# Kernel tuning notes

Hardware: AMD Instinct MI355X
Metric: run time of the kernel (lower is better)

The kernel has to match this reference:

```python
import jax, jax.numpy as jnp
import numpy as np

TOPK = 10
NUM_CLASSES = 80
ALPHA = 0.5
BETA = 6.0
EPS = 1e-9


def setup_inputs() -> dict:
    key = jax.random.key(0)
    ks = jax.random.split(key, 7)
    bs, A, n, C = 16, 8400, 64, NUM_CLASSES
    pd_scores = jax.random.uniform(ks[0], (bs, A, C), jnp.float32)
    # valid xyxy boxes inside a 640x640 image
    pxy = jax.random.uniform(ks[1], (bs, A, 2), jnp.float32) * 576.0
    pwh = jax.random.uniform(ks[2], (bs, A, 2), jnp.float32) * 64.0 + 8.0
    pd_bboxes = jnp.concatenate([pxy, pxy + pwh], axis=-1)
    gxy = jax.random.uniform(ks[3], (bs, n, 2), jnp.float32) * 576.0
    gwh = jax.random.uniform(ks[4], (bs, n, 2), jnp.float32) * 64.0 + 8.0
    gt_bboxes = jnp.concatenate([gxy, gxy + gwh], axis=-1)
    anc_points = jax.random.uniform(ks[5], (A, 2), jnp.float32) * 640.0
    gt_labels = jax.random.randint(ks[6], (bs, n, 1), 0, C, dtype=jnp.int32)
    return {"pd_scores": pd_scores, "pd_bboxes": pd_bboxes,
            "anc_points": anc_points, "gt_labels": gt_labels,
            "gt_bboxes": gt_bboxes}


def _iou(gt_bboxes, pd_bboxes, eps=EPS):
    # gt_bboxes: (bs, n, 4), pd_bboxes: (bs, A, 4) -> (bs, n, A)
    b1 = gt_bboxes[:, :, None, :]
    b2 = pd_bboxes[:, None, :, :]
    lt = jnp.maximum(b1[..., :2], b2[..., :2])
    rb = jnp.minimum(b1[..., 2:], b2[..., 2:])
    overlap = jnp.clip(rb - lt, 0).prod(-1)
    area1 = jnp.clip(b1[..., 2:] - b1[..., :2], 0).prod(-1)
    area2 = jnp.clip(b2[..., 2:] - b2[..., :2], 0).prod(-1)
    return overlap / (area1 + area2 - overlap + eps)


def _assign(pd_scores, pd_bboxes, anc_points, gt_labels, gt_bboxes):
    bs, A, C = pd_scores.shape
    n = gt_bboxes.shape[1]
    dt = pd_scores.dtype
    labels = gt_labels[..., 0]                       # (bs, n)
    # ---- box metrics: gather class score per gt (bs, n, A) ----
    bi = jnp.arange(bs)[:, None]                     # (bs, 1)
    bbox_scores = pd_scores[bi, :, labels]           # (bs, n, A)
    overlaps = _iou(gt_bboxes, pd_bboxes)            # (bs, n, A)
    align_metric = bbox_scores ** ALPHA * overlaps ** BETA
    # ---- anchor-center-in-gt mask ----
    lt = gt_bboxes[..., None, :2]                    # (bs, n, 1, 2)
    rb = gt_bboxes[..., None, 2:]
    anc = anc_points[None, None]                     # (1, 1, A, 2)
    deltas_min = jnp.minimum((anc - lt).min(-1), (rb - anc).min(-1))
    mask_in_gts = (deltas_min > EPS).astype(dt)      # (bs, n, A)
    # ---- top-k candidates per gt (scatter-add instead of huge one-hot) ----
    metrics = align_metric * mask_in_gts
    topk_vals, topk_idxs = jax.lax.top_k(metrics, TOPK)
    valid = topk_vals.max(-1, keepdims=True) > EPS
    topk_idxs = jnp.where(valid, topk_idxs, 0)
    bi3 = jnp.arange(bs)[:, None, None]
    ni3 = jnp.arange(n)[None, :, None]
    cnt = jnp.zeros((bs, n, A), dt).at[bi3, ni3, topk_idxs].add(1.0)
    is_in_topk = jnp.where(cnt > 1, jnp.zeros((), dt), cnt)
    mask_pos = is_in_topk * mask_in_gts
    # ---- resolve anchors assigned to multiple gts via highest IoU ----
    fg_mask = mask_pos.sum(-2)                       # (bs, A)
    mask_multi = fg_mask[:, None, :] > 1             # (bs, 1->n, A)
    is_max = jax.nn.one_hot(overlaps.argmax(1), n, axis=1, dtype=dt)  # (bs, n, A)
    mask_pos = jnp.where(mask_multi, is_max, mask_pos)
    fg_mask = mask_pos.sum(-2)
    target_gt_idx = mask_pos.argmax(-2)              # (bs, A)
    # ---- gather targets ----
    flat_idx = target_gt_idx + jnp.arange(bs)[:, None] * n
    target_labels = jnp.maximum(labels.reshape(-1)[flat_idx], 0)
    target_bboxes = gt_bboxes.reshape(-1, 4)[flat_idx]
    target_scores = jax.nn.one_hot(target_labels, C, dtype=dt)
    target_scores = jnp.where(fg_mask[..., None] > 0, target_scores,
                              jnp.zeros((), dt))
    # ---- normalize scores by task-aligned metric ----
    align_metric = align_metric * mask_pos
    pos_align = align_metric.max(-1, keepdims=True)
    pos_over = (overlaps * mask_pos).max(-1, keepdims=True)
    norm = (align_metric * pos_over / (pos_align + EPS)).max(-2)[..., None]
    target_scores = target_scores * norm
    return target_labels, target_bboxes, target_scores, fg_mask > 0


def reference(pd_scores, pd_bboxes, anc_points, gt_labels, gt_bboxes):
    return _assign(pd_scores, pd_bboxes, anc_points, gt_labels, gt_bboxes)
```

## Files before the change

kernel.cpp:

```cpp
#include <hip/hip_runtime.h>

#define TOPK 10
#define EPSF 1e-9f
#define CHUNKS 8

typedef unsigned long long u64;
typedef unsigned int u32;

__device__ __forceinline__ float gt_area(const float4 g) {
    return fmaxf(g.z - g.x, 0.f) * fmaxf(g.w - g.y, 0.f);
}
__device__ __forceinline__ float iou_pair(const float4 g, const float4 p, float ga) {
    float ow = fmaxf(fminf(g.z, p.z) - fmaxf(g.x, p.x), 0.f) *
               fmaxf(fminf(g.w, p.w) - fmaxf(g.y, p.y), 0.f);
    float pa = fmaxf(p.z - p.x, 0.f) * fmaxf(p.w - p.y, 0.f);
    return ow / (ga + pa - ow + EPSF);
}
__device__ __forceinline__ float dmin_f(const float4 g, const float2 ap) {
    return fminf(fminf(ap.x - g.x, ap.y - g.y), fminf(g.z - ap.x, g.w - ap.y));
}
__device__ __forceinline__ u64 wave_max_u64(u64 v) {
    #pragma unroll
    for (int s = 1; s < 64; s <<= 1) {
        u64 o = __shfl_xor(v, s, 64);
        v = (o > v) ? o : v;
    }
    return v;
}

__global__ __launch_bounds__(256) void k_init(uint4* __restrict__ p, int n16) {
    int i = blockIdx.x * 256 + threadIdx.x;
    if (i < n16) p[i] = make_uint4(0, 0, 0, 0);
}

__global__ __launch_bounds__(256) void k_chunk(
    const float* __restrict__ pd_scores, const float* __restrict__ pd_bboxes,
    const float* __restrict__ anc, const int* __restrict__ gt_labels,
    const float* __restrict__ gt_bboxes, u64* __restrict__ part,
    int A, int n, int C)
{
    const int gw   = blockIdx.x * 4 + (threadIdx.x >> 6);
    const int lane = threadIdx.x & 63;
    const int row  = gw >> 3;
    const int ch   = gw & (CHUNKS - 1);
    const int b    = row / n;
    const int CS   = (A + CHUNKS - 1) / CHUNKS;
    const int a0   = ch * CS;
    const int a1   = min(A, a0 + CS);

    const float4 g = *(const float4*)(gt_bboxes + (size_t)row * 4);
    const int    c = gt_labels[row];
    const float* ps = pd_scores + (size_t)b * A * C + c;
    const float4* pb = (const float4*)(pd_bboxes + (size_t)b * A * 4);
    const float2* an2 = (const float2*)anc;
    const float ga = gt_area(g);

    u64 tk[TOPK];
    #pragma unroll
    for (int k = 0; k < TOPK; ++k) tk[k] = 0;

    for (int a = a0 + lane; a < a1; a += 64) {
        float2 ap = an2[a];
        float dmin = dmin_f(g, ap);
        if (dmin > EPSF) {
            float iou = iou_pair(g, pb[a], ga);
            float met = sqrtf(ps[(size_t)a * C]) * powf(iou, 6.0f);
            if (met > 0.f) {
                u64 key = ((u64)__float_as_uint(met) << 32) | (u32)(0x7fffffff - a);
                if (key > tk[TOPK-1]) {
                    tk[TOPK-1] = key;
                    #pragma unroll
                    for (int k = TOPK-1; k > 0; --k)
                        if (tk[k] > tk[k-1]) { u64 t = tk[k]; tk[k] = tk[k-1]; tk[k-1] = t; }
                }
            }
        }
    }

    u64 mine = 0;
    #pragma unroll
    for (int r = 0; r < TOPK; ++r) {
        u64 m = wave_max_u64(tk[0]);
        if (m == 0) break;
        if (lane == r) mine = m;
        if (tk[0] == m) {
            #pragma unroll
            for (int k = 0; k < TOPK - 1; ++k) tk[k] = tk[k + 1];
            tk[TOPK-1] = 0;
        }
    }
    if (lane < TOPK)
        part[((size_t)row * CHUNKS + ch) * TOPK + lane] = mine;
}

__global__ __launch_bounds__(256) void k_merge(
    const float* __restrict__ pd_scores, const float* __restrict__ pd_bboxes,
    const float* __restrict__ anc, const int* __restrict__ gt_labels,
    const float* __restrict__ gt_bboxes,
    const u64* __restrict__ part, u64* __restrict__ mask64,
    int A, int n, int C)
{
    const int row  = blockIdx.x * 4 + (threadIdx.x >> 6);
    const int lane = threadIdx.x & 63;
    const int b    = row / n;
    const int j    = row - b * n;

    const u64* l = part + (size_t)row * (CHUNKS * TOPK);
    u64 e0 = l[lane];
    u64 e1 = (lane < CHUNKS * TOPK - 64) ? l[64 + lane] : 0;

    const float4 g = *(const float4*)(gt_bboxes + (size_t)row * 4);
    const int    c = gt_labels[row];
    const float* ps = pd_scores + (size_t)b * A * C + c;
    const float4* pb = (const float4*)(pd_bboxes + (size_t)b * A * 4);
    const float2* an2 = (const float2*)anc;
    const float ga = gt_area(g);
    u64* mrow = mask64 + (size_t)b * A;

    int npos = 0;
    bool invalid = false;
    u64 mine = 0;
    for (int r = 0; r < TOPK; ++r) {
        u64 me = (e0 > e1) ? e0 : e1;
        u64 m = wave_max_u64(me);
        if (r == 0) {
            float m0 = __uint_as_float((u32)(m >> 32));
            if (!(m0 > EPSF)) { invalid = true; break; }
        }
        if (m == 0) break;
        if (lane == r) mine = m;
        if (e0 == m) e0 = 0; else if (e1 == m) e1 = 0;
        ++npos;
    }

    if (lane < npos) {
        int a = 0x7fffffff - (int)(u32)(mine & 0xffffffffu);
        if (dmin_f(g, an2[a]) > EPSF)
            atomicOr(&mrow[a], 1ull << j);
    }

    if (!invalid) {
        int need = TOPK - npos;
        int base = 0;
        while (need > 0 && base < A) {
            int a = base + lane;
            float met = 1.f;
            float dmin = -1.f;
            if (a < A) {
                float2 ap = an2[a];
                dmin = dmin_f(g, ap);
                met = 0.f;
                if (dmin > EPSF) {
                    float iou = iou_pair(g, pb[a], ga);
                    met = sqrtf(ps[(size_t)a * C]) * powf(iou, 6.0f);
                }
            }
            u64 zm = __ballot(met == 0.f);
            int cnt = __popcll(zm);
            int take = (need < cnt) ? need : cnt;
            int rank = __popcll(zm & ((1ull << lane) - 1ull));
            if (met == 0.f && rank < take && dmin > EPSF)
                atomicOr(&mrow[a], 1ull << j);
            need -= take;
            base += 64;
        }
    }
}

__global__ __launch_bounds__(256) void k_col(
    const float* __restrict__ pd_scores, const float* __restrict__ pd_bboxes,
    const int* __restrict__ gt_labels, const float* __restrict__ gt_bboxes,
    u64* __restrict__ mask64,
    float* __restrict__ out_labels, float* __restrict__ out_bboxes,
    float* __restrict__ out_fg,
    float* __restrict__ pos_align, float* __restrict__ pos_over,
    int A, int n, int C)
{
    __shared__ float4 sg[64];
    __shared__ int    sl[64];
    const int b = blockIdx.y;
    const int a = blockIdx.x * 256 + threadIdx.x;
    if (threadIdx.x < n) {
        sg[threadIdx.x] = ((const float4*)gt_bboxes)[b * n + threadIdx.x];
        sl[threadIdx.x] = gt_labels[b * n + threadIdx.x];
    }
    __syncthreads();
    if (a >= A) return;

    const size_t midx = (size_t)b * A + a;
    u64 m = mask64[midx];
    int pc = __popcll(m);
    int jt = 0;
    float4 p;
    if (pc) p = ((const float4*)pd_bboxes)[midx];
    if (pc > 1) {
        float bv = iou_pair(sg[0], p, gt_area(sg[0]));
        int bj = 0;
        for (int jj = 1; jj < n; ++jj) {
            float v = iou_pair(sg[jj], p, gt_area(sg[jj]));
            if (v > bv) { bv = v; bj = jj; }
        }
        jt = bj; mask64[midx] = 1ull << bj; pc = 1;
    } else if (pc == 1) {
        jt = __ffsll(m) - 1;
    }

    int lab = sl[jt];
    out_labels[midx] = (float)(lab < 0 ? 0 : lab);
    ((float4*)out_bboxes)[midx] = sg[jt];
    out_fg[midx] = pc ? 1.f : 0.f;

    if (pc) {
        int rowj = b * n + jt;
        float4 gj = sg[jt];
        float iou = iou_pair(gj, p, gt_area(gj));
        float s = pd_scores[midx * C + lab];
        float al = sqrtf(s) * powf(iou, 6.0f);
        atomicMax((int*)&pos_align[rowj], __float_as_int(al));
        atomicMax((int*)&pos_over[rowj],  __float_as_int(iou));
    }
}

__global__ __launch_bounds__(256) void k_norm(
    const float* __restrict__ pd_scores, const float* __restrict__ pd_bboxes,
    const int* __restrict__ gt_labels, const float* __restrict__ gt_bboxes,
    const u64* __restrict__ mask64,
    const float* __restrict__ pos_align, const float* __restrict__ pos_over,
    float* __restrict__ normv, int A, int n, int C, int total)
{
    int idx = blockIdx.x * 256 + threadIdx.x;
    if (idx >= total) return;
    int b = idx / A;
    u64 m = mask64[idx];
    float nm = 0.f;
    if (m) {
        int jt = __ffsll(m) - 1;
        int rowj = b * n + jt;
        float4 gj = *(const float4*)(gt_bboxes + (size_t)rowj * 4);
        float4 p  = ((const float4*)pd_bboxes)[idx];
        float iou = iou_pair(gj, p, gt_area(gj));
        float s = pd_scores[(size_t)idx * C + gt_labels[rowj]];
        float al = sqrtf(s) * powf(iou, 6.0f);
        nm = al * pos_over[rowj] / (pos_align[rowj] + EPSF);
    }
    normv[idx] = nm;
}

__global__ __launch_bounds__(256) void k_scores(
    const float* __restrict__ out_labels, const float* __restrict__ out_fg,
    const float* __restrict__ normv, float4* __restrict__ out_scores,
    int C4, int quads)
{
    int idx = blockIdx.x * 256 + threadIdx.x;
    if (idx >= quads) return;
    int ba = idx / C4;
    int q  = idx - ba * C4;
    float4 v = make_float4(0.f, 0.f, 0.f, 0.f);
    if (out_fg[ba] > 0.f) {
        int r = (int)out_labels[ba] - q * 4;
        float nv = normv[ba];
        v.x = (r == 0) ? nv : 0.f;
        v.y = (r == 1) ? nv : 0.f;
        v.z = (r == 2) ? nv : 0.f;
        v.w = (r == 3) ? nv : 0.f;
    }
    out_scores[idx] = v;
}

extern "C" void kernel_launch(void* const* d_in, const int* in_sizes, int n_in,
                              void* d_out, int out_size, void* d_ws, size_t ws_size,
                              hipStream_t stream)
{
    const float* pd_scores = (const float*)d_in[0];
    const float* pd_bboxes = (const float*)d_in[1];
    const float* anc       = (const float*)d_in[2];
    const int*   gt_labels = (const int*)d_in[3];
    const float* gt_bboxes = (const float*)d_in[4];

    const int C  = 80;
    const int A  = in_sizes[2] / 2;
    const int bs = in_sizes[0] / (A * C);
    const int n  = in_sizes[3] / bs;
    const int R  = bs * n;
    const int BA = bs * A;

    size_t off = 0;
    u64*   mask64    = (u64*)((char*)d_ws + off);   off += (size_t)BA * 8;
    float* pos_align = (float*)((char*)d_ws + off); off += (size_t)R * 4;
    float* pos_over  = (float*)((char*)d_ws + off); off += (size_t)R * 4;
    size_t zero_bytes = off;
    float* normv = (float*)((char*)d_ws + off);     off += (size_t)BA * 4;
    u64*   part  = (u64*)((char*)d_ws + off);       off += (size_t)R * CHUNKS * TOPK * 8;

    float* out_labels = (float*)d_out;
    float* out_bboxes = out_labels + (size_t)BA;
    float* out_scores = out_bboxes + (size_t)BA * 4;
    float* out_fg     = out_scores + (size_t)BA * C;

    int n16 = (int)(zero_bytes / 16);
    k_init<<<(n16 + 255) / 256, 256, 0, stream>>>((uint4*)d_ws, n16);

    k_chunk<<<R * CHUNKS / 4, 256, 0, stream>>>(
        pd_scores, pd_bboxes, anc, gt_labels, gt_bboxes, part, A, n, C);

    k_merge<<<R / 4, 256, 0, stream>>>(
        pd_scores, pd_bboxes, anc, gt_labels, gt_bboxes, part, mask64, A, n, C);

    k_col<<<dim3((A + 255) / 256, bs), 256, 0, stream>>>(
        pd_scores, pd_bboxes, gt_labels, gt_bboxes, mask64,
        out_labels, out_bboxes, out_fg, pos_align, pos_over, A, n, C);

    k_norm<<<(BA + 255) / 256, 256, 0, stream>>>(
        pd_scores, pd_bboxes, gt_labels, gt_bboxes, mask64,
        pos_align, pos_over, normv, A, n, C, BA);

    int quads = BA * (C / 4);
    k_scores<<<(quads + 255) / 256, 256, 0, stream>>>(
        out_labels, out_fg, normv, (float4*)out_scores, C / 4, quads);
}
```

Before: 151.1 us.

## Replace chunked per-gt top-k scan with anchor-major candidate compaction

Instead of each gt row scanning all anchors in chunks with strided score gathers, a per-anchor kernel tests all gts for that anchor, reads its own contiguous score row, and appends positive metrics to a per-gt candidate list via atomics. A second kernel then takes the top-k from each short candidate list and sets mask bits, which removes the separate merge pass. The alignment metric is also cached from k_col so k_norm no longer recomputes IoU and gathers scores. This adds atomic contention on the per-gt counters and a fixed capacity of 1024 candidates, which could drop candidates if a gt ever has more.

```diff
diff --git a/kernel.cpp b/kernel.cpp
--- a/kernel.cpp
+++ b/kernel.cpp
@@ -2,7 +2,7 @@
 
 #define TOPK 10
 #define EPSF 1e-9f
-#define CHUNKS 8
+#define CAP  1024
 
 typedef unsigned long long u64;
 typedef unsigned int u32;
@@ -33,54 +33,84 @@
     if (i < n16) p[i] = make_uint4(0, 0, 0, 0);
 }
 
-__global__ __launch_bounds__(256) void k_chunk(
+__global__ __launch_bounds__(256) void k_cand(
     const float* __restrict__ pd_scores, const float* __restrict__ pd_bboxes,
     const float* __restrict__ anc, const int* __restrict__ gt_labels,
-    const float* __restrict__ gt_bboxes, u64* __restrict__ part,
+    const float* __restrict__ gt_bboxes,
+    u64* __restrict__ cand, int* __restrict__ cnt,
     int A, int n, int C)
 {
-    const int gw   = blockIdx.x * 4 + (threadIdx.x >> 6);
+    __shared__ float4 sg[64];
+    __shared__ float  sga[64];
+    __shared__ int    sl[64];
+    const int b = blockIdx.y;
+    const int a = blockIdx.x * 256 + threadIdx.x;
+    if (threadIdx.x < n) {
+        float4 g4 = ((const float4*)gt_bboxes)[b * n + threadIdx.x];
+        sg[threadIdx.x]  = g4;
+        sga[threadIdx.x] = gt_area(g4);
+        sl[threadIdx.x]  = gt_labels[b * n + threadIdx.x];
+    }
+    __syncthreads();
+    if (a >= A) return;
+
+    const float2 ap = ((const float2*)anc)[a];
+    const float4 p  = ((const float4*)pd_bboxes)[(size_t)b * A + a];
+    const float* psa = pd_scores + ((size_t)b * A + a) * C;
+
+    for (int jj = 0; jj < n; ++jj) {
+        float4 g = sg[jj];
+        float dmin = dmin_f(g, ap);
+        if (dmin > EPSF) {
+            float iou = iou_pair(g, p, sga[jj]);
+            float met = sqrtf(psa[sl[jj]]) * powf(iou, 6.0f);
+            if (met > 0.f) {
+                int row = b * n + jj;
+                u64 key = ((u64)__float_as_uint(met) << 32) | (u32)(0x7fffffff - a);
+                int pos = atomicAdd(&cnt[row], 1);
+                if (pos < CAP) cand[(size_t)row * CAP + pos] = key;
+            }
+        }
+    }
+}
+
+__global__ __launch_bounds__(256) void k_top(
+    const float* __restrict__ pd_scores, const float* __restrict__ pd_bboxes,
+    const float* __restrict__ anc, const int* __restrict__ gt_labels,
+    const float* __restrict__ gt_bboxes,
+    const u64* __restrict__ cand, const int* __restrict__ cnt,
+    u64* __restrict__ mask64, int A, int n, int C)
+{
+    const int row  = blockIdx.x * 4 + (threadIdx.x >> 6);
     const int lane = threadIdx.x & 63;
-    const int row  = gw >> 3;
-    const int ch   = gw & (CHUNKS - 1);
     const int b    = row / n;
-    const int CS   = (A + CHUNKS - 1) / CHUNKS;
-    const int a0   = ch * CS;
-    const int a1   = min(A, a0 + CS);
-
-    const float4 g = *(const float4*)(gt_bboxes + (size_t)row * 4);
-    const int    c = gt_labels[row];
-    const float* ps = pd_scores + (size_t)b * A * C + c;
-    const float4* pb = (const float4*)(pd_bboxes + (size_t)b * A * 4);
-    const float2* an2 = (const float2*)anc;
-    const float ga = gt_area(g);
+    const int j    = row - b * n;
+    const int m_cnt = min(cnt[row], CAP);
+    const u64* cl = cand + (size_t)row * CAP;
 
     u64 tk[TOPK];
     #pragma unroll
     for (int k = 0; k < TOPK; ++k) tk[k] = 0;
-
-    for (int a = a0 + lane; a < a1; a += 64) {
-        float2 ap = an2[a];
-        float dmin = dmin_f(g, ap);
-        if (dmin > EPSF) {
-            float iou = iou_pair(g, pb[a], ga);
-            float met = sqrtf(ps[(size_t)a * C]) * powf(iou, 6.0f);
-            if (met > 0.f) {
-                u64 key = ((u64)__float_as_uint(met) << 32) | (u32)(0x7fffffff - a);
-                if (key > tk[TOPK-1]) {
-                    tk[TOPK-1] = key;
-                    #pragma unroll
-                    for (int k = TOPK-1; k > 0; --k)
-                        if (tk[k] > tk[k-1]) { u64 t = tk[k]; tk[k] = tk[k-1]; tk[k-1] = t; }
-                }
-            }
-        }
-    }
-
+    for (int e = lane; e < m_cnt; e += 64) {
+        u64 key = cl[e];
+        if (key > tk[TOPK-1]) {
+            tk[TOPK-1] = key;
+            #pragma unroll
+            for (int k = TOPK-1; k > 0; --k)
+                if (tk[k] > tk[k-1]) { u64 t = tk[k]; tk[k] = tk[k-1]; tk[k-1] = t; }
+        }
+    }
+
+    int npos = 0;
+    bool invalid = false;
     u64 mine = 0;
     #pragma unroll
     for (int r = 0; r < TOPK; ++r) {
         u64 m = wave_max_u64(tk[0]);
+        if (r == 0) {
+            float m0 = __uint_as_float((u32)(m >> 32));
+            if (!(m0 > EPSF)) { invalid = true; break; }
+        }
         if (m == 0) break;
         if (lane == r) mine = m;
         if (tk[0] == m) {
@@ -88,66 +118,28 @@
             for (int k = 0; k < TOPK - 1; ++k) tk[k] = tk[k + 1];
             tk[TOPK-1] = 0;
         }
-    }
-    if (lane < TOPK)
-        part[((size_t)row * CHUNKS + ch) * TOPK + lane] = mine;
-}
-
-__global__ __launch_bounds__(256) void k_merge(
-    const float* __restrict__ pd_scores, const float* __restrict__ pd_bboxes,
-    const float* __restrict__ anc, const int* __restrict__ gt_labels,
-    const float* __restrict__ gt_bboxes,
-    const u64* __restrict__ part, u64* __restrict__ mask64,
-    int A, int n, int C)
-{
-    const int row  = blockIdx.x * 4 + (threadIdx.x >> 6);
-    const int lane = threadIdx.x & 63;
-    const int b    = row / n;
-    const int j    = row - b * n;
-
-    const u64* l = part + (size_t)row * (CHUNKS * TOPK);
-    u64 e0 = l[lane];
-    u64 e1 = (lane < CHUNKS * TOPK - 64) ? l[64 + lane] : 0;
-
-    const float4 g = *(const float4*)(gt_bboxes + (size_t)row * 4);
-    const int    c = gt_labels[row];
-    const float* ps = pd_scores + (size_t)b * A * C + c;
-    const float4* pb = (const float4*)(pd_bboxes + (size_t)b * A * 4);
-    const float2* an2 = (const float2*)anc;
-    const float ga = gt_area(g);
+        ++npos;
+    }
+
     u64* mrow = mask64 + (size_t)b * A;
-
-    int npos = 0;
-    bool invalid = false;
-    u64 mine = 0;
-    for (int r = 0; r < TOPK; ++r) {
-        u64 me = (e0 > e1) ? e0 : e1;
-        u64 m = wave_max_u64(me);
-        if (r == 0) {
-            float m0 = __uint_as_float((u32)(m >> 32));
-            if (!(m0 > EPSF)) { invalid = true; break; }
-        }
-        if (m == 0) break;
-        if (lane == r) mine = m;
-        if (e0 == m) e0 = 0; else if (e1 == m) e1 = 0;
-        ++npos;
-    }
-
     if (lane < npos) {
         int a = 0x7fffffff - (int)(u32)(mine & 0xffffffffu);
-        if (dmin_f(g, an2[a]) > EPSF)
-            atomicOr(&mrow[a], 1ull << j);
-    }
-
-    if (!invalid) {
+        atomicOr(&mrow[a], 1ull << j);
+    }
+    if (!invalid && npos < TOPK) {
+        const float4 g = *(const float4*)(gt_bboxes + (size_t)row * 4);
+        const float ga = gt_area(g);
+        const int   c  = gt_labels[row];
+        const float* ps = pd_scores + (size_t)b * A * C + c;
+        const float4* pb = (const float4*)(pd_bboxes + (size_t)b * A * 4);
         int need = TOPK - npos;
         int base = 0;
         while (need > 0 && base < A) {
-            int a = base + lane;
+            const int a = base + lane;
             float met = 1.f;
             float dmin = -1.f;
             if (a < A) {
-                float2 ap = an2[a];
+                float2 ap = ((const float2*)anc)[a];
                 dmin = dmin_f(g, ap);
                 met = 0.f;
                 if (dmin > EPSF) {
@@ -156,8 +148,8 @@
                 }
             }
             u64 zm = __ballot(met == 0.f);
-            int cnt = __popcll(zm);
-            int take = (need < cnt) ? need : cnt;
+            int cntz = __popcll(zm);
+            int take = (need < cntz) ? need : cntz;
             int rank = __popcll(zm & ((1ull << lane) - 1ull));
             if (met == 0.f && rank < take && dmin > EPSF)
                 atomicOr(&mrow[a], 1ull << j);
@@ -172,7 +164,7 @@
     const int* __restrict__ gt_labels, const float* __restrict__ gt_bboxes,
     u64* __restrict__ mask64,
     float* __restrict__ out_labels, float* __restrict__ out_bboxes,
-    float* __restrict__ out_fg,
+    float* __restrict__ out_fg, float* __restrict__ alv,
     float* __restrict__ pos_align, float* __restrict__ pos_over,
     int A, int n, int C)
 {
@@ -216,17 +208,16 @@
         float iou = iou_pair(gj, p, gt_area(gj));
         float s = pd_scores[midx * C + lab];
         float al = sqrtf(s) * powf(iou, 6.0f);
+        alv[midx] = al;
         atomicMax((int*)&pos_align[rowj], __float_as_int(al));
         atomicMax((int*)&pos_over[rowj],  __float_as_int(iou));
     }
 }
 
 __global__ __launch_bounds__(256) void k_norm(
-    const float* __restrict__ pd_scores, const float* __restrict__ pd_bboxes,
-    const int* __restrict__ gt_labels, const float* __restrict__ gt_bboxes,
-    const u64* __restrict__ mask64,
+    const u64* __restrict__ mask64, const float* __restrict__ alv,
     const float* __restrict__ pos_align, const float* __restrict__ pos_over,
-    float* __restrict__ normv, int A, int n, int C, int total)
+    float* __restrict__ normv, int A, int n, int total)
 {
     int idx = blockIdx.x * 256 + threadIdx.x;
     if (idx >= total) return;
@@ -234,14 +225,8 @@
     u64 m = mask64[idx];
     float nm = 0.f;
     if (m) {
-        int jt = __ffsll(m) - 1;
-        int rowj = b * n + jt;
-        float4 gj = *(const float4*)(gt_bboxes + (size_t)rowj * 4);
-        float4 p  = ((const float4*)pd_bboxes)[idx];
-        float iou = iou_pair(gj, p, gt_area(gj));
-        float s = pd_scores[(size_t)idx * C + gt_labels[rowj]];
-        float al = sqrtf(s) * powf(iou, 6.0f);
-        nm = al * pos_over[rowj] / (pos_align[rowj] + EPSF);
+        int rowj = b * n + (__ffsll(m) - 1);
+        nm = alv[idx] * pos_over[rowj] / (pos_align[rowj] + EPSF);
     }
     normv[idx] = nm;
 }
@@ -288,9 +273,11 @@
     u64*   mask64    = (u64*)((char*)d_ws + off);   off += (size_t)BA * 8;
     float* pos_align = (float*)((char*)d_ws + off); off += (size_t)R * 4;
     float* pos_over  = (float*)((char*)d_ws + off); off += (size_t)R * 4;
+    int*   cand_cnt  = (int*)((char*)d_ws + off);   off += (size_t)R * 4;
     size_t zero_bytes = off;
+    float* alv   = (float*)((char*)d_ws + off);     off += (size_t)BA * 4;
     float* normv = (float*)((char*)d_ws + off);     off += (size_t)BA * 4;
-    u64*   part  = (u64*)((char*)d_ws + off);       off += (size_t)R * CHUNKS * TOPK * 8;
+    u64*   cand  = (u64*)((char*)d_ws + off);       off += (size_t)R * CAP * 8;
 
     float* out_labels = (float*)d_out;
     float* out_bboxes = out_labels + (size_t)BA;
@@ -300,19 +287,19 @@
     int n16 = (int)(zero_bytes / 16);
     k_init<<<(n16 + 255) / 256, 256, 0, stream>>>((uint4*)d_ws, n16);
 
-    k_chunk<<<R * CHUNKS / 4, 256, 0, stream>>>(
-        pd_scores, pd_bboxes, anc, gt_labels, gt_bboxes, part, A, n, C);
-
-    k_merge<<<R / 4, 256, 0, stream>>>(
-        pd_scores, pd_bboxes, anc, gt_labels, gt_bboxes, part, mask64, A, n, C);
+    k_cand<<<dim3((A + 255) / 256, bs), 256, 0, stream>>>(
+        pd_scores, pd_bboxes, anc, gt_labels, gt_bboxes, cand, cand_cnt, A, n, C);
+
+    k_top<<<R / 4, 256, 0, stream>>>(
+        pd_scores, pd_bboxes, anc, gt_labels, gt_bboxes, cand, cand_cnt,
+        mask64, A, n, C);
 
     k_col<<<dim3((A + 255) / 256, bs), 256, 0, stream>>>(
         pd_scores, pd_bboxes, gt_labels, gt_bboxes, mask64,
-        out_labels, out_bboxes, out_fg, pos_align, pos_over, A, n, C);
+        out_labels, out_bboxes, out_fg, alv, pos_align, pos_over, A, n, C);
 
     k_norm<<<(BA + 255) / 256, 256, 0, stream>>>(
-        pd_scores, pd_bboxes, gt_labels, gt_bboxes, mask64,
-        pos_align, pos_over, normv, A, n, C, BA);
+        mask64, alv, pos_align, pos_over, normv, A, n, BA);
 
     int quads = BA * (C / 4);
     k_scores<<<(quads + 255) / 256, 256, 0, stream>>>(
```

Result: faster. 147.4 us (-2.5%).
